# Kernel tuning notes

Measured on AMD Instinct MI355X. Metric: run time of the kernel, lower is better.

Reference implementation:

```python
import jax, jax.numpy as jnp
import numpy as np

IN_FEATURES = 4096
OUT_FEATURES = 4096
NUM_GROUPS = 16
GROUP_IN = IN_FEATURES // NUM_GROUPS    # 256
GROUP_OUT = OUT_FEATURES // NUM_GROUPS  # 256
BATCH = 8192


def setup_inputs() -> dict:
    key = jax.random.key(0)
    kx, kw, kb = jax.random.split(key, 3)
    x = jax.random.normal(kx, (BATCH, IN_FEATURES), dtype=jnp.float32)
    # nn.Linear weight is [out, in]; stack per-group -> [G, dout_g, din_g]
    bound = 1.0 / np.sqrt(GROUP_IN)
    W = jax.random.uniform(kw, (NUM_GROUPS, GROUP_OUT, GROUP_IN), dtype=jnp.float32,
                           minval=-bound, maxval=bound)
    b = jax.random.uniform(kb, (NUM_GROUPS, GROUP_OUT), dtype=jnp.float32,
                           minval=-bound, maxval=bound)
    return {"x": x, "W": W, "b": b}


def reference(x, W, b):
    B = x.shape[0]
    # split along features -> [B, G, din_g]; block-diagonal matmul as batched GEMM
    xg = x.reshape(B, NUM_GROUPS, GROUP_IN)
    # y[b,g,o] = sum_i xg[b,g,i] * W[g,o,i] + b[g,o]
    yg = jnp.einsum('bgi,goi->bgo', xg, W) + b
    return yg.reshape(B, OUT_FEATURES)
```

## Files before the change

kernel.cpp:

```cpp
#include <hip/hip_runtime.h>
#include <hip/hip_bf16.h>
#include <stdint.h>


#define IN_F   4096
#define OUT_F  4096
#define GIN    256
#define GOUT   256

#define BM 128
#define BN 128
#define BK 64
#define KTOT 256

using short8  = __attribute__((ext_vector_type(8))) short;
using floatx4 = __attribute__((ext_vector_type(4))) float;

__device__ __forceinline__ short f2bf_rne(float f) {
    unsigned u = __builtin_bit_cast(unsigned, f);
    unsigned r = u + 0x7FFFu + ((u >> 16) & 1u);
    return (short)(r >> 16);
}

__global__ __launch_bounds__(256, 2)
void grouped_linear_kernel(const float* __restrict__ X,
                           const float* __restrict__ W,
                           const float* __restrict__ Bias,
                           float* __restrict__ Out) {
    __shared__ __align__(16) short lsA[BM * BK];
    __shared__ __align__(16) short lsB[BN * BK];

    const int t    = threadIdx.x;
    const int lane = t & 63;
    const int wave = t >> 6;
    const int wm   = wave >> 1;
    const int wn   = wave & 1;
    const int lrow = lane & 15;
    const int quad = lane >> 4;

    const int bn   = blockIdx.x & 31;
    const int bm   = blockIdx.x >> 5;
    const int g    = bn >> 1;
    const int row0 = bm * BM;
    const int col0 = bn * BN;
    const int nlb  = (bn & 1) * BN;

    const float* Wg = W + (size_t)g * GOUT * GIN + (size_t)nlb * GIN;
    const float* Xg = X + (size_t)row0 * IN_F + g * GIN;

    floatx4 acc[4][4];
    #pragma unroll
    for (int i = 0; i < 4; ++i)
        #pragma unroll
        for (int j = 0; j < 4; ++j)
            acc[i][j] = (floatx4){0.f, 0.f, 0.f, 0.f};

    const int c8 = (t & 7) * 8;
    const int q0 = (t & 7);

    for (int kt = 0; kt < KTOT / BK; ++kt) {
        const int kbase = kt * BK;

        #pragma unroll
        for (int i = 0; i < 4; ++i) {
            int r = (t >> 3) + 32 * i;
            const float* src = Xg + (size_t)r * IN_F + kbase + c8;
            floatx4 f0 = *(const floatx4*)src;
            floatx4 f1 = *(const floatx4*)(src + 4);
            short8 p;
            p[0] = f2bf_rne(f0[0]); p[1] = f2bf_rne(f0[1]);
            p[2] = f2bf_rne(f0[2]); p[3] = f2bf_rne(f0[3]);
            p[4] = f2bf_rne(f1[0]); p[5] = f2bf_rne(f1[1]);
            p[6] = f2bf_rne(f1[2]); p[7] = f2bf_rne(f1[3]);
            int q = q0 ^ (r & 7);
            *(short8*)&lsA[r * BK + q * 8] = p;
        }
        #pragma unroll
        for (int i = 0; i < 4; ++i) {
            int n = (t >> 3) + 32 * i;
            const float* src = Wg + (size_t)n * GIN + kbase + c8;
            floatx4 f0 = *(const floatx4*)src;
            floatx4 f1 = *(const floatx4*)(src + 4);
            short8 p;
            p[0] = f2bf_rne(f0[0]); p[1] = f2bf_rne(f0[1]);
            p[2] = f2bf_rne(f0[2]); p[3] = f2bf_rne(f0[3]);
            p[4] = f2bf_rne(f1[0]); p[5] = f2bf_rne(f1[1]);
            p[6] = f2bf_rne(f1[2]); p[7] = f2bf_rne(f1[3]);
            int q = q0 ^ (n & 7);
            *(short8*)&lsB[n * BK + q * 8] = p;
        }
        __syncthreads();

        #pragma unroll
        for (int kk = 0; kk < 2; ++kk) {
            int kb = kk * 32 + quad * 8;
            int qs = kb >> 3;
            short8 a[4], b[4];
            #pragma unroll
            for (int i = 0; i < 4; ++i) {
                int r = wm * 64 + i * 16 + lrow;
                a[i] = *(const short8*)&lsA[r * BK + ((qs ^ (r & 7)) * 8)];
            }
            #pragma unroll
            for (int j = 0; j < 4; ++j) {
                int n = wn * 64 + j * 16 + lrow;
                b[j] = *(const short8*)&lsB[n * BK + ((qs ^ (n & 7)) * 8)];
            }
            #pragma unroll
            for (int i = 0; i < 4; ++i)
                #pragma unroll
                for (int j = 0; j < 4; ++j)
                    acc[i][j] = __builtin_amdgcn_mfma_f32_16x16x32_bf16(
                        a[i], b[j], acc[i][j], 0, 0, 0);
        }
        __syncthreads();
    }

    #pragma unroll
    for (int j = 0; j < 4; ++j) {
        int gc = col0 + wn * 64 + j * 16 + lrow;
        float bias = Bias[gc];
        #pragma unroll
        for (int i = 0; i < 4; ++i) {
            int gr = row0 + wm * 64 + i * 16 + quad * 4;
            floatx4 v = acc[i][j];
            #pragma unroll
            for (int rg = 0; rg < 4; ++rg)
                Out[(size_t)(gr + rg) * OUT_F + gc] = v[rg] + bias;
        }
    }
}

extern "C" void kernel_launch(void* const* d_in, const int* in_sizes, int n_in,
                              void* d_out, int out_size, void* d_ws, size_t ws_size,
                              hipStream_t stream) {
    const float* X    = (const float*)d_in[0];
    const float* W    = (const float*)d_in[1];
    const float* Bias = (const float*)d_in[2];
    float*       Out  = (float*)d_out;

    dim3 grid(64 * 32);
    dim3 block(256);
    grouped_linear_kernel<<<grid, block, 0, stream>>>(X, W, Bias, Out);
}
```

Before: 272.2 us.

## Remap blocks per XCD for L2 locality and use lighter LDS barriers

```diff
diff --git a/kernel.cpp b/kernel.cpp
--- a/kernel.cpp
+++ b/kernel.cpp
@@ -1,5 +1,4 @@
 #include <hip/hip_runtime.h>
-#include <hip/hip_bf16.h>
 #include <stdint.h>
 
 
@@ -22,7 +21,23 @@
     return (short)(r >> 16);
 }
 
-__global__ __launch_bounds__(256, 2)
+__device__ __forceinline__ short8 pack8(floatx4 f0, floatx4 f1) {
+    short8 p;
+    p[0] = f2bf_rne(f0[0]); p[1] = f2bf_rne(f0[1]);
+    p[2] = f2bf_rne(f0[2]); p[3] = f2bf_rne(f0[3]);
+    p[4] = f2bf_rne(f1[0]); p[5] = f2bf_rne(f1[1]);
+    p[6] = f2bf_rne(f1[2]); p[7] = f2bf_rne(f1[3]);
+    return p;
+}
+
+#define SYNC_PHASE() do {                                        \
+    asm volatile("s_waitcnt lgkmcnt(0)" ::: "memory");           \
+    __builtin_amdgcn_sched_barrier(0);                           \
+    __builtin_amdgcn_s_barrier();                                \
+    __builtin_amdgcn_sched_barrier(0);                           \
+} while (0)
+
+__global__ __launch_bounds__(256) __attribute__((amdgpu_waves_per_eu(4)))
 void grouped_linear_kernel(const float* __restrict__ X,
                            const float* __restrict__ W,
                            const float* __restrict__ Bias,
@@ -38,8 +53,15 @@
     const int lrow = lane & 15;
     const int quad = lane >> 4;
 
-    const int bn   = blockIdx.x & 31;
-    const int bm   = blockIdx.x >> 5;
+    const int bid   = blockIdx.x;
+    const int xcd   = bid & 7;
+    const int idx   = bid >> 3;
+    const int bmblk = idx >> 5;
+    const int bn_l  = (idx >> 3) & 3;
+    const int bm_i  = idx & 7;
+    const int bn    = xcd * 4 + bn_l;
+    const int bm    = bmblk * 8 + bm_i;
+
     const int g    = bn >> 1;
     const int row0 = bm * BM;
     const int col0 = bn * BN;
@@ -57,44 +79,34 @@
 
     const int c8 = (t & 7) * 8;
     const int q0 = (t & 7);
+    const int r0 = (t >> 3);
 
     for (int kt = 0; kt < KTOT / BK; ++kt) {
         const int kbase = kt * BK;
 
         #pragma unroll
-        for (int i = 0; i < 4; ++i) {
-            int r = (t >> 3) + 32 * i;
+        for (int it = 0; it < 4; ++it) {
+            int r = r0 + 32 * it;
             const float* src = Xg + (size_t)r * IN_F + kbase + c8;
             floatx4 f0 = *(const floatx4*)src;
             floatx4 f1 = *(const floatx4*)(src + 4);
-            short8 p;
-            p[0] = f2bf_rne(f0[0]); p[1] = f2bf_rne(f0[1]);
-            p[2] = f2bf_rne(f0[2]); p[3] = f2bf_rne(f0[3]);
-            p[4] = f2bf_rne(f1[0]); p[5] = f2bf_rne(f1[1]);
-            p[6] = f2bf_rne(f1[2]); p[7] = f2bf_rne(f1[3]);
             int q = q0 ^ (r & 7);
-            *(short8*)&lsA[r * BK + q * 8] = p;
+            *(short8*)&lsA[r * BK + q * 8] = pack8(f0, f1);
         }
         #pragma unroll
-        for (int i = 0; i < 4; ++i) {
-            int n = (t >> 3) + 32 * i;
+        for (int it = 0; it < 4; ++it) {
+            int n = r0 + 32 * it;
             const float* src = Wg + (size_t)n * GIN + kbase + c8;
             floatx4 f0 = *(const floatx4*)src;
             floatx4 f1 = *(const floatx4*)(src + 4);
-            short8 p;
-            p[0] = f2bf_rne(f0[0]); p[1] = f2bf_rne(f0[1]);
-            p[2] = f2bf_rne(f0[2]); p[3] = f2bf_rne(f0[3]);
-            p[4] = f2bf_rne(f1[0]); p[5] = f2bf_rne(f1[1]);
-            p[6] = f2bf_rne(f1[2]); p[7] = f2bf_rne(f1[3]);
             int q = q0 ^ (n & 7);
-            *(short8*)&lsB[n * BK + q * 8] = p;
+            *(short8*)&lsB[n * BK + q * 8] = pack8(f0, f1);
         }
-        __syncthreads();
+        SYNC_PHASE();
 
         #pragma unroll
         for (int kk = 0; kk < 2; ++kk) {
-            int kb = kk * 32 + quad * 8;
-            int qs = kb >> 3;
+            int qs = kk * 4 + quad;
             short8 a[4], b[4];
             #pragma unroll
             for (int i = 0; i < 4; ++i) {
@@ -113,7 +125,7 @@
                     acc[i][j] = __builtin_amdgcn_mfma_f32_16x16x32_bf16(
                         a[i], b[j], acc[i][j], 0, 0, 0);
         }
-        __syncthreads();
+        SYNC_PHASE();
     }
 
     #pragma unroll
```

Result: faster. 265.4 us (-2.5%).
